# Performance work log

Measured on AMD Instinct MI355X. Metric: run time of the kernel, lower is better.

## Reference

```python
import jax, jax.numpy as jnp
import numpy as np

WIN = 20  # patch_project window_size
HID = 128


def _lstm_layer(x, w_ih, w_hh, b_ih, b_hh):
    """x: [B,T,D] -> (outputs [B,T,H], final h [B,H]). PyTorch gate order i,f,g,o."""
    B = x.shape[0]
    H = w_hh.shape[1]
    # precompute input contribution for all timesteps: [B,T,4H]
    x_pre = jnp.einsum('btd,gd->btg', x, w_ih) + b_ih + b_hh

    def step(carry, xp):
        h, c = carry
        gates = xp + h @ w_hh.T  # [B,4H]
        i, f, g, o = jnp.split(gates, 4, axis=-1)
        i = jax.nn.sigmoid(i)
        f = jax.nn.sigmoid(f)
        g = jnp.tanh(g)
        o = jax.nn.sigmoid(o)
        c = f * c + i * g
        h = o * jnp.tanh(c)
        return (h, c), h

    h0 = jnp.zeros((B, H), x.dtype)
    c0 = jnp.zeros((B, H), x.dtype)
    (h_f, _), ys = jax.lax.scan(step, (h0, c0), x_pre.transpose(1, 0, 2))
    return ys.transpose(1, 0, 2), h_f


def setup_inputs() -> dict:
    key = jax.random.key(0)
    ks = jax.random.split(key, 20)
    B, S, C = 64, 2048, 32
    D_in = WIN * C          # 640
    D_p = D_in // 2         # 320
    H = HID
    label_len = 48
    s = 0.02
    inp = {
        'inputs': jax.random.normal(ks[0], (B, S, C), jnp.float32),
        '_x': jnp.zeros((B, 4), jnp.float32),
        'y': jnp.zeros((B, label_len), jnp.float32),
        '_y': jnp.zeros((B, 4), jnp.float32),
        'proj_w': jax.random.normal(ks[1], (D_p, D_in), jnp.float32) * s,
        'proj_b': jax.random.normal(ks[2], (D_p,), jnp.float32) * s,
        'w_ih0': jax.random.normal(ks[3], (4 * H, D_p), jnp.float32) * s,
        'w_hh0': jax.random.normal(ks[4], (4 * H, H), jnp.float32) * s,
        'b_ih0': jax.random.normal(ks[5], (4 * H,), jnp.float32) * s,
        'b_hh0': jax.random.normal(ks[6], (4 * H,), jnp.float32) * s,
        'w_ih_rest': jax.random.normal(ks[7], (3, 4 * H, H), jnp.float32) * s,
        'w_hh_rest': jax.random.normal(ks[8], (3, 4 * H, H), jnp.float32) * s,
        'b_ih_rest': jax.random.normal(ks[9], (3, 4 * H), jnp.float32) * s,
        'b_hh_rest': jax.random.normal(ks[10], (3, 4 * H), jnp.float32) * s,
        'out_w': jax.random.normal(ks[11], (label_len, H), jnp.float32) * s,
        'out_b': jax.random.normal(ks[12], (label_len,), jnp.float32) * s,
    }
    return inp


def reference(inputs, _x, y, _y, proj_w, proj_b, w_ih0, w_hh0, b_ih0, b_hh0,
              w_ih_rest, w_hh_rest, b_ih_rest, b_hh_rest, out_w, out_b):
    B, S, C = inputs.shape
    L_out = S - WIN
    idx = jnp.arange(L_out)[:, None] + jnp.arange(WIN)[None, :]
    windows = inputs[:, idx, :].reshape(B, L_out, WIN * C)
    # projection1 (dropout is inference no-op)
    x = jnp.einsum('btd,pd->btp', windows, proj_w) + proj_b
    # 4-layer LSTM (dropout between layers is inference no-op)
    x, h = _lstm_layer(x, w_ih0, w_hh0, b_ih0, b_hh0)
    for l in range(3):
        x, h = _lstm_layer(x, w_ih_rest[l], w_hh_rest[l], b_ih_rest[l], b_hh_rest[l])
    # final hidden state of last layer -> [B,1,H] -> output layer -> [B,1,label_len]
    out = h[:, None, :] @ out_w.T + out_b
    return out
```

## Files before the change

kernel.cpp:

```cpp
#include <hip/hip_runtime.h>
#include <stdint.h>
#include <stddef.h>

typedef __bf16 bf16_t;
typedef bf16_t bf16x8 __attribute__((ext_vector_type(8)));
typedef bf16_t bf16x4 __attribute__((ext_vector_type(4)));
typedef float  f32x4  __attribute__((ext_vector_type(4)));

#define T_STEPS 2028
#define SEQ     2048
#define CIN     32
#define NG      32
#define MB      2
#define CH      32
#define NCH     64
#define RING    4

#define OFF_EFFW   0u
#define OFF_BIAS   655360u
#define OFF_WHH    663552u
#define OFF_WIH    1187840u
#define OFF_HFIN   1581056u
#define OFF_CNT    1613824u
#define OFF_XRING  1638400u
#define OFF_YRING  35192832u

__device__ __forceinline__ int endk(int k) {
  int e = (k + 1) * CH;
  return e > T_STEPS ? T_STEPS : e;
}

__device__ __forceinline__ void spin_ge(uint32_t* p, uint32_t tgt) {
  while (atomicAdd(p, 0u) < tgt) __builtin_amdgcn_s_sleep(2);
}
__device__ __forceinline__ void publish(uint32_t* p, uint32_t v) {
  __builtin_amdgcn_fence(__ATOMIC_RELEASE, "agent");
  atomicMax(p, v);
}

__device__ __forceinline__ float fsigm(float x) {
  return __builtin_amdgcn_rcpf(1.0f + __builtin_amdgcn_exp2f(x * -1.44269504089f));
}
__device__ __forceinline__ float ftanh(float x) {
  return 1.0f - 2.0f * __builtin_amdgcn_rcpf(1.0f + __builtin_amdgcn_exp2f(x * 2.88539008178f));
}

__device__ __forceinline__ bf16x8 ldg8(const bf16_t* p) { return *(const bf16x8*)p; }
__device__ __forceinline__ bf16x4 ldg4(const bf16_t* p) { return *(const bf16x4*)p; }

__device__ __forceinline__ bf16x8 ldg_cvt8(const float* p) {
  const f32x4 a = *(const f32x4*)p;
  const f32x4 b = *(const f32x4*)(p + 4);
  bf16x8 r;
  r[0] = (bf16_t)a[0]; r[1] = (bf16_t)a[1]; r[2] = (bf16_t)a[2]; r[3] = (bf16_t)a[3];
  r[4] = (bf16_t)b[0]; r[5] = (bf16_t)b[1]; r[6] = (bf16_t)b[2]; r[7] = (bf16_t)b[3];
  return r;
}


__global__ void k_prep_misc(const float* __restrict__ w_hh0,
                            const float* __restrict__ w_ih_rest,
                            const float* __restrict__ w_hh_rest,
                            const float* __restrict__ b_ih_rest,
                            const float* __restrict__ b_hh_rest,
                            uint8_t* __restrict__ ws) {
  const int bid = blockIdx.x;
  const int l = bid >> 9;
  const int p = bid & 511;
  const int orig = (p & 3) * 128 + (p >> 2);
  const int tid = threadIdx.x;
  bf16_t* whh = (bf16_t*)(ws + OFF_WHH);
  bf16_t* wih = (bf16_t*)(ws + OFF_WIH);
  float* bias = (float*)(ws + OFF_BIAS);
  const float* src = (l == 0) ? (w_hh0 + orig * 128)
                              : (w_hh_rest + ((size_t)(l - 1) * 512 + orig) * 128);
  whh[((size_t)l * 512 + p) * 128 + tid] = (bf16_t)src[tid];
  if (l < 3)
    wih[((size_t)l * 512 + p) * 128 + tid] = (bf16_t)w_ih_rest[((size_t)l * 512 + orig) * 128 + tid];
  if (l >= 1 && tid == 0)
    bias[l * 512 + p] = b_ih_rest[(l - 1) * 512 + orig] + b_hh_rest[(l - 1) * 512 + orig];
  if (bid == 0) {
    uint32_t* cnt = (uint32_t*)(ws + OFF_CNT);
    for (int i = tid; i < 12 * 32 * 16; i += 128) cnt[i] = 0;
  }
}

__global__ void k_prep_effw(const float* __restrict__ proj_w,
                            const float* __restrict__ proj_b,
                            const float* __restrict__ w_ih0,
                            const float* __restrict__ b_ih0,
                            const float* __restrict__ b_hh0,
                            uint8_t* __restrict__ ws) {
  __shared__ float wr[320];
  const int p = blockIdx.x;
  const int orig = (p & 3) * 128 + (p >> 2);
  const int tid = threadIdx.x;
  for (int i = tid; i < 320; i += 256) wr[i] = w_ih0[(size_t)orig * 320 + i];
  __syncthreads();
  bf16_t* effw = (bf16_t*)(ws + OFF_EFFW);
  for (int kk = tid; kk < 640; kk += 256) {
    float a = 0.f;
    for (int z = 0; z < 320; ++z) a += wr[z] * proj_w[(size_t)z * 640 + kk];
    effw[(size_t)p * 640 + kk] = (bf16_t)a;
  }
  if (tid == 0) {
    float a = 0.f;
    for (int z = 0; z < 320; ++z) a += wr[z] * proj_b[z];
    ((float*)(ws + OFF_BIAS))[p] = a + b_ih0[orig] + b_hh0[orig];
  }
}

__global__ __launch_bounds__(256, 1) void k_pipeline(const float* __restrict__ in,
                                                     uint8_t* __restrict__ ws) {
  __shared__ __align__(16) bf16_t h_lds[2][16][136];
  __shared__ f32x4 gate_buf[4][2][32];

  const int s = blockIdx.x >> 5;
  const int g = blockIdx.x & 31;
  const int tid = threadIdx.x;
  const int lane = tid & 63;
  const int w = tid >> 6;
  const int q = lane >> 4;
  const int ln = lane & 15;

  uint32_t* cnt = (uint32_t*)(ws + OFF_CNT);
  bf16_t* xring = (bf16_t*)(ws + OFF_XRING);
  bf16_t* yring = (bf16_t*)(ws + OFF_YRING);

  if (s == 0) {
    const bf16_t* effw = (const bf16_t*)(ws + OFF_EFFW);
    uint32_t* my = cnt + (0 * NG + g) * 16;
    uint32_t* guard = cnt + (1 * NG + g) * 16;
    for (int k = 0; k < NCH; ++k) {
      if (tid == 0 && k >= RING) spin_ge(guard, (uint32_t)endk(k - RING));
      __syncthreads();
      const int t0 = k * CH;
      f32x4 acc[4][8];
#pragma unroll
      for (int mt = 0; mt < 4; ++mt)
#pragma unroll
        for (int nt = 0; nt < 8; ++nt) acc[mt][nt] = (f32x4){0.f, 0.f, 0.f, 0.f};
#pragma unroll
      for (int kt = 0; kt < 20; ++kt) {
        bf16x8 bfr[8];
#pragma unroll
        for (int nt = 0; nt < 8; ++nt)
          bfr[nt] = ldg8(effw + (size_t)((w * 8 + nt) * 16 + ln) * 640 + kt * 32 + q * 8);
#pragma unroll
        for (int mt = 0; mt < 4; ++mt) {
          int m = mt * 16 + ln;
          int trel = m >> 1, bb = m & 1;
          int tt = t0 + trel; if (tt > T_STEPS - 1) tt = T_STEPS - 1;
          bf16x8 afr = ldg_cvt8(in + (size_t)((g * MB + bb) * SEQ + tt + kt) * CIN + q * 8);
#pragma unroll
          for (int nt = 0; nt < 8; ++nt)
            acc[mt][nt] = __builtin_amdgcn_mfma_f32_16x16x32_bf16(afr, bfr[nt], acc[mt][nt], 0, 0, 0);
        }
      }
      bf16_t* xs = xring + (size_t)((0 * NG + g) * RING + (k & 3)) * (64 * 512);
#pragma unroll
      for (int mt = 0; mt < 4; ++mt)
#pragma unroll
        for (int nt = 0; nt < 8; ++nt)
#pragma unroll
          for (int r = 0; r < 4; ++r)
            xs[(size_t)(mt * 16 + q * 4 + r) * 512 + (w * 8 + nt) * 16 + ln] = (bf16_t)acc[mt][nt][r];
      __syncthreads();
      if (tid == 0) publish(my, (uint32_t)endk(k));
    }
  } else if (s <= 4) {
    const int l = s - 1;
    const bf16_t* whh = (const bf16_t*)(ws + OFF_WHH) + (size_t)l * 512 * 128;
    bf16x8 wfr[8][4];
#pragma unroll
    for (int mt = 0; mt < 8; ++mt)
#pragma unroll
      for (int kt = 0; kt < 4; ++kt)
        wfr[mt][kt] = ldg8(whh + (size_t)(w * 128 + mt * 16 + ln) * 128 + kt * 32 + q * 8);
    const int b_ep = lane >> 5;
    const int j_loc = lane & 31;
    const int jg = w * 32 + j_loc;
    f32x4 biasq = *(const f32x4*)((const float*)(ws + OFF_BIAS) + l * 512 + 4 * jg);
    float c = 0.f;
    {
      bf16_t* hz = &h_lds[0][0][0];
      for (int i = tid; i < 2 * 16 * 136; i += 256) hz[i] = (bf16_t)0.f;
    }
    __syncthreads();
    uint32_t* my = cnt + ((1 + l) * NG + g) * 16;
    uint32_t* prod = (l == 0) ? (cnt + (0 * NG + g) * 16) : (cnt + ((4 + l) * NG + g) * 16);
    uint32_t* yguard = cnt + ((5 + l) * NG + g) * 16;
    float* hfin = (float*)(ws + OFF_HFIN);
    const int ly = (l < 3) ? l : 0;

    for (int k = 0; k < NCH; ++k) {
      const int t0 = k * CH;
      const int tlen = (T_STEPS - t0 < CH) ? (T_STEPS - t0) : CH;
      if (tid == 0) {
        spin_ge(prod, (uint32_t)(t0 + tlen));
        if (l < 3 && k >= RING) spin_ge(yguard, (uint32_t)endk(k - RING));
        __builtin_amdgcn_fence(__ATOMIC_ACQUIRE, "agent");
      }
      __syncthreads();
      const bf16_t* xlane = xring + (size_t)((l * NG + g) * RING + (k & 3)) * (64 * 512)
                            + b_ep * 512 + 4 * jg;
      bf16_t* ylane = yring + (size_t)((ly * NG + g) * RING + (k & 3)) * (64 * 128)
                      + b_ep * 128 + jg;
      bf16x4 xq[4];
#pragma unroll
      for (int i = 0; i < 4; ++i) xq[i] = ldg4(xlane + i * 1024);
      for (int trel = 0; trel < tlen; trel += 4) {
#pragma unroll
        for (int i = 0; i < 4; ++i) {
          const int t = t0 + trel + i;
          const int buf = t & 1;
          f32x4 acc[8];
#pragma unroll
          for (int mt = 0; mt < 8; ++mt) acc[mt] = (f32x4){0.f, 0.f, 0.f, 0.f};
#pragma unroll
          for (int kt = 0; kt < 4; ++kt) {
            bf16x8 hk = *(const bf16x8*)&h_lds[buf][ln][kt * 32 + q * 8];
#pragma unroll
            for (int mt = 0; mt < 8; ++mt)
              acc[mt] = __builtin_amdgcn_mfma_f32_16x16x32_bf16(wfr[mt][kt], hk, acc[mt], 0, 0, 0);
          }
          if (ln < MB) {
#pragma unroll
            for (int mt = 0; mt < 8; ++mt)
              gate_buf[w][ln][mt * 4 + q] = acc[mt];
          }
          f32x4 gq = gate_buf[w][b_ep][j_loc];
          float gi = fsigm(gq[0] + (float)xq[i][0] + biasq[0]);
          float gf = fsigm(gq[1] + (float)xq[i][1] + biasq[1]);
          float gg = ftanh(gq[2] + (float)xq[i][2] + biasq[2]);
          float go = fsigm(gq[3] + (float)xq[i][3] + biasq[3]);
          c = gf * c + gi * gg;
          float hv = go * ftanh(c);
          const int tn = trel + i + 4;
          if (tn < tlen) xq[i] = ldg4(xlane + tn * 1024);
          h_lds[buf ^ 1][b_ep][jg] = (bf16_t)hv;
          if (l < 3) ylane[(size_t)(trel + i) * 256] = (bf16_t)hv;
          if (l == 3 && t == T_STEPS - 1) hfin[(g * MB + b_ep) * 128 + jg] = hv;
          asm volatile("s_waitcnt lgkmcnt(0)\n\ts_barrier" ::: "memory");
        }
      }
      __syncthreads();
      if (tid == 0) publish(my, (uint32_t)(t0 + tlen));
    }
  } else {
    const int l = s - 4;
    const bf16_t* wih = (const bf16_t*)(ws + OFF_WIH) + (size_t)(l - 1) * 512 * 128;
    bf16x8 bfr[8][4];
#pragma unroll
    for (int nt = 0; nt < 8; ++nt)
#pragma unroll
      for (int kt = 0; kt < 4; ++kt)
        bfr[nt][kt] = ldg8(wih + (size_t)((w * 8 + nt) * 16 + ln) * 128 + kt * 32 + q * 8);
    uint32_t* my = cnt + ((4 + l) * NG + g) * 16;
    uint32_t* prod = cnt + (l * NG + g) * 16;
    uint32_t* xguard = cnt + ((1 + l) * NG + g) * 16;
    for (int k = 0; k < NCH; ++k) {
      if (tid == 0) {
        spin_ge(prod, (uint32_t)endk(k));
        if (k >= RING) spin_ge(xguard, (uint32_t)endk(k - RING));
        __builtin_amdgcn_fence(__ATOMIC_ACQUIRE, "agent");
      }
      __syncthreads();
      const bf16_t* ys = yring + (size_t)(((l - 1) * NG + g) * RING + (k & 3)) * (64 * 128);
      bf16_t* xs = xring + (size_t)((l * NG + g) * RING + (k & 3)) * (64 * 512);
#pragma unroll
      for (int mt = 0; mt < 4; ++mt) {
        f32x4 a8[8];
#pragma unroll
        for (int nt = 0; nt < 8; ++nt) a8[nt] = (f32x4){0.f, 0.f, 0.f, 0.f};
#pragma unroll
        for (int kt = 0; kt < 4; ++kt) {
          bf16x8 afr = ldg8(ys + (size_t)(mt * 16 + ln) * 128 + kt * 32 + q * 8);
#pragma unroll
          for (int nt = 0; nt < 8; ++nt)
            a8[nt] = __builtin_amdgcn_mfma_f32_16x16x32_bf16(afr, bfr[nt][kt], a8[nt], 0, 0, 0);
        }
#pragma unroll
        for (int nt = 0; nt < 8; ++nt)
#pragma unroll
          for (int r = 0; r < 4; ++r)
            xs[(size_t)(mt * 16 + q * 4 + r) * 512 + (w * 8 + nt) * 16 + ln] = (bf16_t)a8[nt][r];
      }
      __syncthreads();
      if (tid == 0) publish(my, (uint32_t)endk(k));
    }
  }
}

__global__ void k_out(const float* __restrict__ out_w,
                      const float* __restrict__ out_b,
                      const uint8_t* __restrict__ ws,
                      float* __restrict__ out) {
  const int idx = blockIdx.x * 256 + threadIdx.x;
  const int b = idx / 48, o = idx % 48;
  const float* h = (const float*)(ws + OFF_HFIN) + b * 128;
  const float* wrow = out_w + (size_t)o * 128;
  float a = out_b[o];
  for (int j = 0; j < 128; ++j) a += h[j] * wrow[j];
  out[idx] = a;
}

extern "C" void kernel_launch(void* const* d_in, const int* in_sizes, int n_in,
                              void* d_out, int out_size, void* d_ws, size_t ws_size,
                              hipStream_t stream) {
  (void)in_sizes; (void)n_in; (void)out_size; (void)ws_size;
  const float* inputs    = (const float*)d_in[0];
  const float* proj_w    = (const float*)d_in[4];
  const float* proj_b    = (const float*)d_in[5];
  const float* w_ih0     = (const float*)d_in[6];
  const float* w_hh0     = (const float*)d_in[7];
  const float* b_ih0     = (const float*)d_in[8];
  const float* b_hh0     = (const float*)d_in[9];
  const float* w_ih_rest = (const float*)d_in[10];
  const float* w_hh_rest = (const float*)d_in[11];
  const float* b_ih_rest = (const float*)d_in[12];
  const float* b_hh_rest = (const float*)d_in[13];
  const float* out_w     = (const float*)d_in[14];
  const float* out_b     = (const float*)d_in[15];
  uint8_t* ws = (uint8_t*)d_ws;
  float* out = (float*)d_out;

  k_prep_misc<<<dim3(2048), dim3(128), 0, stream>>>(w_hh0, w_ih_rest, w_hh_rest,
                                                    b_ih_rest, b_hh_rest, ws);
  k_prep_effw<<<dim3(512), dim3(256), 0, stream>>>(proj_w, proj_b, w_ih0, b_ih0, b_hh0, ws);
  k_pipeline<<<dim3(256), dim3(256), 0, stream>>>(inputs, ws);
  k_out<<<dim3(12), dim3(256), 0, stream>>>(out_w, out_b, ws, out);
}
```

Measured before the change: 2.932 ms.

## Run LSTM recurrence on two waves with 16 gate tiles each, batch x/y I/O

The recurrent-step work per block moves from four waves with 8 MFMA tiles each to two waves with 16 tiles each. Each active lane now owns one hidden unit for both batch rows, and the two idle waves only mirror the per-step barriers. The x loads are hoisted in groups of 8 steps and the y stores are batched after each group. The input-projection stage also preloads all A fragments before its MFMA loop. This aims to cut barrier and LDS coordination cost per serial timestep, but doubles MFMA and register load per active wave, which risks spilling 64 weight fragments.

```diff
diff --git a/kernel.cpp b/kernel.cpp
--- a/kernel.cpp
+++ b/kernel.cpp
@@ -113,7 +113,7 @@
 __global__ __launch_bounds__(256, 1) void k_pipeline(const float* __restrict__ in,
                                                      uint8_t* __restrict__ ws) {
   __shared__ __align__(16) bf16_t h_lds[2][16][136];
-  __shared__ f32x4 gate_buf[4][2][32];
+  __shared__ f32x4 gbuf[2][2][64];
 
   const int s = blockIdx.x >> 5;
   const int g = blockIdx.x & 31;
@@ -170,82 +170,135 @@
     }
   } else if (s <= 4) {
     const int l = s - 1;
-    const bf16_t* whh = (const bf16_t*)(ws + OFF_WHH) + (size_t)l * 512 * 128;
-    bf16x8 wfr[8][4];
-#pragma unroll
-    for (int mt = 0; mt < 8; ++mt)
-#pragma unroll
-      for (int kt = 0; kt < 4; ++kt)
-        wfr[mt][kt] = ldg8(whh + (size_t)(w * 128 + mt * 16 + ln) * 128 + kt * 32 + q * 8);
-    const int b_ep = lane >> 5;
-    const int j_loc = lane & 31;
-    const int jg = w * 32 + j_loc;
-    f32x4 biasq = *(const f32x4*)((const float*)(ws + OFF_BIAS) + l * 512 + 4 * jg);
-    float c = 0.f;
     {
       bf16_t* hz = &h_lds[0][0][0];
       for (int i = tid; i < 2 * 16 * 136; i += 256) hz[i] = (bf16_t)0.f;
     }
     __syncthreads();
-    uint32_t* my = cnt + ((1 + l) * NG + g) * 16;
-    uint32_t* prod = (l == 0) ? (cnt + (0 * NG + g) * 16) : (cnt + ((4 + l) * NG + g) * 16);
-    uint32_t* yguard = cnt + ((5 + l) * NG + g) * 16;
-    float* hfin = (float*)(ws + OFF_HFIN);
-    const int ly = (l < 3) ? l : 0;
-
-    for (int k = 0; k < NCH; ++k) {
-      const int t0 = k * CH;
-      const int tlen = (T_STEPS - t0 < CH) ? (T_STEPS - t0) : CH;
-      if (tid == 0) {
-        spin_ge(prod, (uint32_t)(t0 + tlen));
-        if (l < 3 && k >= RING) spin_ge(yguard, (uint32_t)endk(k - RING));
-        __builtin_amdgcn_fence(__ATOMIC_ACQUIRE, "agent");
-      }
-      __syncthreads();
-      const bf16_t* xlane = xring + (size_t)((l * NG + g) * RING + (k & 3)) * (64 * 512)
-                            + b_ep * 512 + 4 * jg;
-      bf16_t* ylane = yring + (size_t)((ly * NG + g) * RING + (k & 3)) * (64 * 128)
-                      + b_ep * 128 + jg;
-      bf16x4 xq[4];
-#pragma unroll
-      for (int i = 0; i < 4; ++i) xq[i] = ldg4(xlane + i * 1024);
-      for (int trel = 0; trel < tlen; trel += 4) {
-#pragma unroll
-        for (int i = 0; i < 4; ++i) {
-          const int t = t0 + trel + i;
-          const int buf = t & 1;
-          f32x4 acc[8];
-#pragma unroll
-          for (int mt = 0; mt < 8; ++mt) acc[mt] = (f32x4){0.f, 0.f, 0.f, 0.f};
-#pragma unroll
-          for (int kt = 0; kt < 4; ++kt) {
-            bf16x8 hk = *(const bf16x8*)&h_lds[buf][ln][kt * 32 + q * 8];
-#pragma unroll
-            for (int mt = 0; mt < 8; ++mt)
-              acc[mt] = __builtin_amdgcn_mfma_f32_16x16x32_bf16(wfr[mt][kt], hk, acc[mt], 0, 0, 0);
+
+    if (w < 2) {
+      const bf16_t* whh = (const bf16_t*)(ws + OFF_WHH) + (size_t)l * 512 * 128;
+      bf16x8 wfr[16][4];
+#pragma unroll
+      for (int mt = 0; mt < 16; ++mt)
+#pragma unroll
+        for (int kt = 0; kt < 4; ++kt)
+          wfr[mt][kt] = ldg8(whh + (size_t)(w * 256 + mt * 16 + ln) * 128 + kt * 32 + q * 8);
+      const int j = (w << 6) | lane;
+      f32x4 biasq = *(const f32x4*)((const float*)(ws + OFF_BIAS) + l * 512 + 4 * j);
+      float c0 = 0.f, c1 = 0.f;
+      uint32_t* my = cnt + ((1 + l) * NG + g) * 16;
+      uint32_t* prod = (l == 0) ? (cnt + (0 * NG + g) * 16) : (cnt + ((4 + l) * NG + g) * 16);
+      uint32_t* yguard = cnt + ((5 + l) * NG + g) * 16;
+      float* hfin = (float*)(ws + OFF_HFIN);
+      const int ly = (l < 3) ? l : 0;
+
+      auto do_step = [&](int t, bf16x4 x0, bf16x4 x1, bf16_t& y0, bf16_t& y1) {
+        const int buf = t & 1;
+        f32x4 acc[16];
+#pragma unroll
+        for (int mt = 0; mt < 16; ++mt) acc[mt] = (f32x4){0.f, 0.f, 0.f, 0.f};
+#pragma unroll
+        for (int kt = 0; kt < 4; ++kt) {
+          bf16x8 hk = *(const bf16x8*)&h_lds[buf][ln][kt * 32 + q * 8];
+#pragma unroll
+          for (int mt = 0; mt < 16; ++mt)
+            acc[mt] = __builtin_amdgcn_mfma_f32_16x16x32_bf16(wfr[mt][kt], hk, acc[mt], 0, 0, 0);
+        }
+        if (ln < 2) {
+#pragma unroll
+          for (int mt = 0; mt < 16; ++mt) gbuf[w][ln][mt * 4 + q] = acc[mt];
+        }
+        f32x4 g0 = gbuf[w][0][lane];
+        f32x4 g1 = gbuf[w][1][lane];
+        float i0 = fsigm(g0[0] + (float)x0[0] + biasq[0]);
+        float f0 = fsigm(g0[1] + (float)x0[1] + biasq[1]);
+        float z0 = ftanh(g0[2] + (float)x0[2] + biasq[2]);
+        float o0 = fsigm(g0[3] + (float)x0[3] + biasq[3]);
+        c0 = f0 * c0 + i0 * z0;
+        float h0 = o0 * ftanh(c0);
+        float i1 = fsigm(g1[0] + (float)x1[0] + biasq[0]);
+        float f1 = fsigm(g1[1] + (float)x1[1] + biasq[1]);
+        float z1 = ftanh(g1[2] + (float)x1[2] + biasq[2]);
+        float o1 = fsigm(g1[3] + (float)x1[3] + biasq[3]);
+        c1 = f1 * c1 + i1 * z1;
+        float h1 = o1 * ftanh(c1);
+        h_lds[buf ^ 1][0][j] = (bf16_t)h0;
+        h_lds[buf ^ 1][1][j] = (bf16_t)h1;
+        y0 = (bf16_t)h0; y1 = (bf16_t)h1;
+        if (l == 3 && t == T_STEPS - 1) {
+          hfin[(g * MB + 0) * 128 + j] = h0;
+          hfin[(g * MB + 1) * 128 + j] = h1;
+        }
+        asm volatile("s_waitcnt lgkmcnt(0)\n\ts_barrier" ::: "memory");
+      };
+
+      for (int k = 0; k < NCH; ++k) {
+        const int t0 = k * CH;
+        const int tlen = (T_STEPS - t0 < CH) ? (T_STEPS - t0) : CH;
+        if (tid == 0) {
+          spin_ge(prod, (uint32_t)(t0 + tlen));
+          if (l < 3 && k >= RING) spin_ge(yguard, (uint32_t)endk(k - RING));
+          __builtin_amdgcn_fence(__ATOMIC_ACQUIRE, "agent");
+        }
+        __syncthreads();
+        const bf16_t* xl0 = xring + (size_t)((l * NG + g) * RING + (k & 3)) * (64 * 512) + 4 * j;
+        const bf16_t* xl1 = xl0 + 512;
+        bf16_t* yl = yring + (size_t)((ly * NG + g) * RING + (k & 3)) * (64 * 128) + j;
+
+        for (int tq = 0; tq < tlen; tq += 8) {
+          const int qlen = (tlen - tq >= 8) ? 8 : (tlen - tq);
+          if (qlen == 8) {
+            bf16x4 xq0[8], xq1[8];
+#pragma unroll
+            for (int i = 0; i < 8; ++i) {
+              xq0[i] = ldg4(xl0 + (size_t)(tq + i) * 1024);
+              xq1[i] = ldg4(xl1 + (size_t)(tq + i) * 1024);
+            }
+            bf16_t yv0[8], yv1[8];
+#pragma unroll
+            for (int i = 0; i < 8; ++i) do_step(t0 + tq + i, xq0[i], xq1[i], yv0[i], yv1[i]);
+            if (l < 3) {
+#pragma unroll
+              for (int i = 0; i < 8; ++i) {
+                yl[(size_t)(tq + i) * 256] = yv0[i];
+                yl[(size_t)(tq + i) * 256 + 128] = yv1[i];
+              }
+            }
+          } else {
+            bf16x4 xq0[4], xq1[4];
+#pragma unroll
+            for (int i = 0; i < 4; ++i) {
+              xq0[i] = ldg4(xl0 + (size_t)(tq + i) * 1024);
+              xq1[i] = ldg4(xl1 + (size_t)(tq + i) * 1024);
+            }
+            bf16_t yv0[4], yv1[4];
+#pragma unroll
+            for (int i = 0; i < 4; ++i) do_step(t0 + tq + i, xq0[i], xq1[i], yv0[i], yv1[i]);
+            if (l < 3) {
+#pragma unroll
+              for (int i = 0; i < 4; ++i) {
+                yl[(size_t)(tq + i) * 256] = yv0[i];
+                yl[(size_t)(tq + i) * 256 + 128] = yv1[i];
+              }
+            }
           }
-          if (ln < MB) {
-#pragma unroll
-            for (int mt = 0; mt < 8; ++mt)
-              gate_buf[w][ln][mt * 4 + q] = acc[mt];
-          }
-          f32x4 gq = gate_buf[w][b_ep][j_loc];
-          float gi = fsigm(gq[0] + (float)xq[i][0] + biasq[0]);
-          float gf = fsigm(gq[1] + (float)xq[i][1] + biasq[1]);
-          float gg = ftanh(gq[2] + (float)xq[i][2] + biasq[2]);
-          float go = fsigm(gq[3] + (float)xq[i][3] + biasq[3]);
-          c = gf * c + gi * gg;
-          float hv = go * ftanh(c);
-          const int tn = trel + i + 4;
-          if (tn < tlen) xq[i] = ldg4(xlane + tn * 1024);
-          h_lds[buf ^ 1][b_ep][jg] = (bf16_t)hv;
-          if (l < 3) ylane[(size_t)(trel + i) * 256] = (bf16_t)hv;
-          if (l == 3 && t == T_STEPS - 1) hfin[(g * MB + b_ep) * 128 + jg] = hv;
-          asm volatile("s_waitcnt lgkmcnt(0)\n\ts_barrier" ::: "memory");
-        }
-      }
-      __syncthreads();
-      if (tid == 0) publish(my, (uint32_t)(t0 + tlen));
+        }
+        __syncthreads();
+        if (tid == 0) publish(my, (uint32_t)(t0 + tlen));
+      }
+    } else {
+      for (int k = 0; k < NCH; ++k) {
+        const int t0 = k * CH;
+        const int tlen = (T_STEPS - t0 < CH) ? (T_STEPS - t0) : CH;
+        __syncthreads();
+        for (int tq = 0; tq < tlen; tq += 8) {
+          const int qlen = (tlen - tq >= 8) ? 8 : (tlen - tq);
+          for (int i = 0; i < qlen; ++i)
+            asm volatile("s_barrier" ::: "memory");
+        }
+        __syncthreads();
+      }
     }
   } else {
     const int l = s - 4;
@@ -268,6 +321,12 @@
       __syncthreads();
       const bf16_t* ys = yring + (size_t)(((l - 1) * NG + g) * RING + (k & 3)) * (64 * 128);
       bf16_t* xs = xring + (size_t)((l * NG + g) * RING + (k & 3)) * (64 * 512);
+      bf16x8 afr[4][4];
+#pragma unroll
+      for (int mt = 0; mt < 4; ++mt)
+#pragma unroll
+        for (int kt = 0; kt < 4; ++kt)
+          afr[mt][kt] = ldg8(ys + (size_t)(mt * 16 + ln) * 128 + kt * 32 + q * 8);
 #pragma unroll
       for (int mt = 0; mt < 4; ++mt) {
         f32x4 a8[8];
@@ -275,10 +334,9 @@
         for (int nt = 0; nt < 8; ++nt) a8[nt] = (f32x4){0.f, 0.f, 0.f, 0.f};
 #pragma unroll
         for (int kt = 0; kt < 4; ++kt) {
-          bf16x8 afr = ldg8(ys + (size_t)(mt * 16 + ln) * 128 + kt * 32 + q * 8);
 #pragma unroll
           for (int nt = 0; nt < 8; ++nt)
-            a8[nt] = __builtin_amdgcn_mfma_f32_16x16x32_bf16(afr, bfr[nt][kt], a8[nt], 0, 0, 0);
+            a8[nt] = __builtin_amdgcn_mfma_f32_16x16x32_bf16(afr[mt][kt], bfr[nt][kt], a8[nt], 0, 0, 0);
         }
 #pragma unroll
         for (int nt = 0; nt < 8; ++nt)
```

Measured after the change: 3.108 ms. 6.0% more time.
